# Performance work log

Hardware: AMD Instinct MI355X
Metric: run time of the kernel (lower is better)

Reference implementation:

```python
import jax, jax.numpy as jnp
import numpy as np

HUMAN_SIZE = 54
NUM_ACTIONS = 15
INPUT_SIZE = HUMAN_SIZE + NUM_ACTIONS  # 69
RNN_SIZE = 2048
BATCH = 512
SRC_LEN = 100
TGT_LEN = 50


def setup_inputs() -> dict:
    key = jax.random.key(0)
    ks = jax.random.split(key, 8)
    s = 1.0 / np.sqrt(RNN_SIZE)
    return {
        "encoder_inputs": jax.random.normal(ks[0], (BATCH, SRC_LEN, INPUT_SIZE), jnp.float32),
        "decoder_inputs": jax.random.normal(ks[1], (BATCH, TGT_LEN, INPUT_SIZE), jnp.float32),
        # GRUCell params (torch layout: weight_ih [3H, D], weight_hh [3H, H])
        "W_ih": jax.random.uniform(ks[2], (3 * RNN_SIZE, INPUT_SIZE), jnp.float32, -s, s),
        "W_hh": jax.random.uniform(ks[3], (3 * RNN_SIZE, RNN_SIZE), jnp.float32, -s, s),
        "b_ih": jax.random.uniform(ks[4], (3 * RNN_SIZE,), jnp.float32, -s, s),
        "b_hh": jax.random.uniform(ks[5], (3 * RNN_SIZE,), jnp.float32, -s, s),
        # fc1: Linear(rnn_size -> input_size)
        "fc1_w": jax.random.uniform(ks[6], (INPUT_SIZE, RNN_SIZE), jnp.float32, -s, s),
        "fc1_b": jax.random.uniform(ks[7], (INPUT_SIZE,), jnp.float32, -s, s),
    }


def _gru_cell(x, h, W_ih, W_hh, b_ih, b_hh):
    # torch.nn.GRUCell math
    gi = x @ W_ih.T + b_ih  # [B, 3H]
    gh = h @ W_hh.T + b_hh  # [B, 3H]
    i_r, i_z, i_n = jnp.split(gi, 3, axis=-1)
    h_r, h_z, h_n = jnp.split(gh, 3, axis=-1)
    r = jax.nn.sigmoid(i_r + h_r)
    z = jax.nn.sigmoid(i_z + h_z)
    n = jnp.tanh(i_n + r * h_n)
    return (1.0 - z) * n + z * h


def reference(encoder_inputs, decoder_inputs, W_ih, W_hh, b_ih, b_hh, fc1_w, fc1_b):
    B = encoder_inputs.shape[0]
    state0 = jnp.zeros((B, RNN_SIZE), encoder_inputs.dtype)

    # Encoder: source_seq_len - 1 steps (dropout p=0.0 -> identity)
    enc_t = jnp.swapaxes(encoder_inputs[:, : SRC_LEN - 1], 0, 1)  # [L-1, B, D]

    def enc_step(h, x):
        return _gru_cell(x, h, W_ih, W_hh, b_ih, b_hh), None

    state, _ = jax.lax.scan(enc_step, state0, enc_t)

    # (loop_function feeds the previous output back as the next input).
    def dec_step(carry, _):
        h, inp = carry
        inp = jax.lax.stop_gradient(inp)  # inp.detach() in torch
        h = _gru_cell(inp, h, W_ih, W_hh, b_ih, b_hh)
        out = inp + h @ fc1_w.T + fc1_b  # residual
        return (h, out), out

    (_, _), outs = jax.lax.scan(dec_step, (state, decoder_inputs[:, 0]), None, length=TGT_LEN)
    return jnp.swapaxes(outs, 0, 1)  # [B, TGT_LEN, INPUT_SIZE]
```

## Files before the change

kernel.cpp:

```cpp
#include <hip/hip_runtime.h>

#define KP   2176
#define H    2048
#define IN   69
#define TGT  50
#define NKT  68

typedef unsigned short ushort_t;
typedef unsigned int   uint_t;
typedef __attribute__((ext_vector_type(8))) short  short8;
typedef __attribute__((ext_vector_type(4))) float  float4_t;

#define MFMA_BF16 __builtin_amdgcn_mfma_f32_16x16x32_bf16

__device__ __forceinline__ ushort_t f2bf(float f) {
  union { float f; unsigned u; } v; v.f = f;
  unsigned u = v.u;
  return (ushort_t)((u + 0x7fffu + ((u >> 16) & 1u)) >> 16);
}

template <int N> __device__ __forceinline__ void waitv() {
  asm volatile("s_waitcnt vmcnt(%0)" :: "n"(N) : "memory");
}
#define LGKM0() asm volatile("s_waitcnt lgkmcnt(0)" ::: "memory")
#define SGB0()  __builtin_amdgcn_sched_barrier(0)
#define FENCE() asm volatile("" ::: "memory")

template <int OFF> __device__ __forceinline__ void gld(short8& d, uint_t voff, const void* base) {
  asm volatile("global_load_dwordx4 %0, %1, %2 offset:%3"
               : "=v"(d) : "v"(voff), "s"(base), "n"(OFF));
}


__global__ void build_w3(const float* __restrict__ Whh, const float* __restrict__ Wih,
                         ushort_t* __restrict__ W3) {
  int i = blockIdx.x * 256 + threadIdx.x;
  int lane = i & 63;
  int kt = (i >> 6) % NKT;
  int rb = i / (64 * NKT);
  int cb = rb / 3, g = rb - cb * 3;
  int c  = cb * 16 + (lane & 15);
  int gr = g * H + c;
  int k0 = kt * 32 + (lane >> 4) * 8;
  short8 v;
  #pragma unroll
  for (int j = 0; j < 8; ++j) {
    int k = k0 + j;
    float val = 0.f;
    if (k < H) val = Whh[(size_t)gr * H + k];
    else if (k < H + IN) val = Wih[(size_t)gr * IN + (k - H)];
    v[j] = (short)f2bf(val);
  }
  *(short8*)(W3 + (size_t)i * 8) = v;
}

__global__ void build_f2(const float* __restrict__ fc1w, ushort_t* __restrict__ F2) {
  int i = blockIdx.x * 256 + threadIdx.x;
  int lane = i & 63;
  int ni = (i >> 6) % 5;
  int kt = i / 320;
  int j  = ni * 16 + (lane & 15);
  int k0 = kt * 32 + (lane >> 4) * 8;
  short8 v;
  #pragma unroll
  for (int jj = 0; jj < 8; ++jj) {
    float val = (j < IN) ? fc1w[(size_t)j * H + k0 + jj] : 0.f;
    v[jj] = (short)f2bf(val);
  }
  *(short8*)(F2 + (size_t)i * 8) = v;
}

__global__ void zero_u4(uint4* p, int n) {
  int i = blockIdx.x * 256 + threadIdx.x;
  if (i < n) p[i] = make_uint4(0, 0, 0, 0);
}

__device__ __forceinline__ size_t a2_x_off(int b, int j) {
  int k = 2048 + j;
  int kt = k >> 5, kk = k & 31;
  int mb = b >> 4;
  int ln = (b & 15) | ((kk >> 3) << 4);
  return ((size_t)(mb * NKT + kt) * 64 + ln) * 16 + (kk & 7) * 2;
}

__global__ void fill_x0(const float* __restrict__ enc, char* __restrict__ A2) {
  int i = blockIdx.x * 256 + threadIdx.x;
  int b = i / IN, j = i - b * IN;
  *(ushort_t*)(A2 + a2_x_off(b, j)) = f2bf(enc[(size_t)b * 100 * IN + j]);
}

__global__ __launch_bounds__(256, 1) void gru_step(
    const char* __restrict__ Aprev, char* __restrict__ Anext,
    const char* __restrict__ W3p, float* __restrict__ h32,
    const float* __restrict__ bih, const float* __restrict__ bhh,
    const float* __restrict__ xsrc, int xstride)
{
  __shared__ short8  Aring[4][4][64];
  __shared__ ushort_t smh[64][72];
  __shared__ char ldspad[64000];

  const int tid = threadIdx.x;
  const int bid = blockIdx.x;
  const int lane = tid & 63, w = tid >> 6;
  const int l15 = lane & 15, l4 = lane >> 4;
  const int cg = (bid & 7) * 4 + ((bid >> 3) & 3);
  const int mt = bid >> 5;
  const int cb = cg * 4 + w;
  const int c  = cb * 16 + l15;

  if (xstride == -12345) ldspad[tid] = 1;

  const float br  = bih[c] + bhh[c];
  const float bz  = bih[H + c] + bhh[H + c];
  const float bin = bih[2 * H + c];
  const float bhn = bhh[2 * H + c];
  asm volatile("" :: "v"(br), "v"(bz), "v"(bin), "v"(bhn));

  const void* ApW = Aprev + (size_t)(mt * 4) * (NKT * 1024);
  uint_t vA  = (uint_t)(w * (NKT * 1024) + lane * 16);
  uint_t vB0 = (uint_t)((cb * 3 + 0) * (NKT * 1024) + lane * 16);
  uint_t vB1 = (uint_t)((cb * 3 + 1) * (NKT * 1024) + lane * 16);
  uint_t vB2 = (uint_t)((cb * 3 + 2) * (NKT * 1024) + lane * 16);

  short8 sa[4], fb[8][3];
  short8 fa0, fa1, fa2, fa3;
  float4_t acc[4][4] = {};

#define AISS(sl) { gld<0>(sa[sl], vA, ApW); vA += 1024; }
#define BISS(sl) { gld<0>(fb[sl][0], vB0, W3p); gld<0>(fb[sl][1], vB1, W3p); \
                   gld<0>(fb[sl][2], vB2, W3p); vB0 += 1024; vB1 += 1024; vB2 += 1024; }
#define MFMA3(mi, fav, j, G2) \
  acc[mi][0]  = MFMA_BF16(fav, fb[j][0], acc[mi][0], 0, 0, 0); \
  acc[mi][1]  = MFMA_BF16(fav, fb[j][1], acc[mi][1], 0, 0, 0); \
  acc[mi][G2] = MFMA_BF16(fav, fb[j][2], acc[mi][G2], 0, 0, 0);
#define MFMA12(j, G2) MFMA3(0, fa0, j, G2) MFMA3(1, fa1, j, G2) \
                      MFMA3(2, fa2, j, G2) MFMA3(3, fa3, j, G2)
#define RDFA(slot) \
  FENCE(); \
  fa0 = Aring[slot][0][lane]; fa1 = Aring[slot][1][lane]; \
  fa2 = Aring[slot][2][lane]; fa3 = Aring[slot][3][lane];

#define GRUT(u, G2) \
  AISS((u + 4) & 3) BISS((u + 7) & 7) \
  waitv<15>(); SGB0(); \
  Aring[(u + 1) & 3][w][lane] = sa[(u + 1) & 3]; \
  LGKM0(); \
  __builtin_amdgcn_s_barrier(); \
  RDFA(u & 3) \
  LGKM0(); SGB0(); \
  MFMA12(u, G2)

#define GRUTA(u, NW) \
  AISS((u + 4) & 3) \
  waitv<NW>(); SGB0(); \
  Aring[(u + 1) & 3][w][lane] = sa[(u + 1) & 3]; \
  LGKM0(); \
  __builtin_amdgcn_s_barrier(); \
  RDFA(u & 3) \
  LGKM0(); SGB0(); \
  MFMA12(u, 2)

#define GRUTN_W(u, NW, G2) \
  waitv<NW>(); SGB0(); \
  Aring[(u + 1) & 3][w][lane] = sa[(u + 1) & 3]; \
  LGKM0(); \
  __builtin_amdgcn_s_barrier(); \
  RDFA(u & 3) \
  LGKM0(); SGB0(); \
  MFMA12(u, G2)
#define GRUTN_NW(u, NW, G2) \
  waitv<NW>(); SGB0(); \
  LGKM0(); \
  __builtin_amdgcn_s_barrier(); \
  RDFA(u & 3) \
  LGKM0(); SGB0(); \
  MFMA12(u, G2)

  AISS(0) AISS(1) AISS(2) AISS(3)
  BISS(0) BISS(1) BISS(2) BISS(3) BISS(4) BISS(5) BISS(6)
  waitv<24>(); SGB0();
  Aring[0][w][lane] = sa[0];
  LGKM0();
  __builtin_amdgcn_s_barrier();

  #pragma unroll 1
  for (int g8 = 0; g8 < 7; ++g8) {
    GRUT(0, 2) GRUT(1, 2) GRUT(2, 2) GRUT(3, 2)
    GRUT(4, 2) GRUT(5, 2) GRUT(6, 2) GRUT(7, 2)
  }
  GRUT(0, 2) GRUT(1, 2) GRUT(2, 2) GRUT(3, 2) GRUT(4, 2)
  GRUTA(5, 12) GRUTA(6, 9) GRUTA(7, 6)
  GRUTN_W(0, 2, 3) GRUTN_W(1, 1, 3) GRUTN_W(2, 0, 3) GRUTN_NW(3, 0, 3)

  #pragma unroll
  for (int mi = 0; mi < 4; ++mi) {
    #pragma unroll
    for (int r4 = 0; r4 < 4; ++r4) {
      int m = mt * 64 + mi * 16 + l4 * 4 + r4;
      float rg = 1.f / (1.f + __expf(-(acc[mi][0][r4] + br)));
      float zg = 1.f / (1.f + __expf(-(acc[mi][1][r4] + bz)));
      float ng = tanhf(acc[mi][3][r4] + bin + rg * (acc[mi][2][r4] + bhn));
      float hold = h32[(size_t)m * H + c];
      float hn = (1.f - zg) * ng + zg * hold;
      h32[(size_t)m * H + c] = hn;
      smh[mi * 16 + l4 * 4 + r4][w * 16 + l15] = f2bf(hn);
    }
  }
  __syncthreads();
  #pragma unroll
  for (int e = 0; e < 2; ++e) {
    int cid = tid * 2 + e;
    int m = cid >> 3, ktrel = (cid >> 2) & 1, khi = cid & 3;
    short8 v = *(const short8*)&smh[m][ktrel * 32 + khi * 8];
    int m_abs = mt * 64 + m;
    int mb2 = m_abs >> 4;
    int ln = (m_abs & 15) | (khi << 4);
    int kt = cg * 2 + ktrel;
    *(short8*)(Anext + ((size_t)(mb2 * NKT + kt) * 64 + ln) * 16) = v;
  }
  if ((bid & 31) == 0 && xsrc != nullptr) {
    for (int i = tid; i < 64 * IN; i += 256) {
      int rr = i / IN, cc = i - rr * IN;
      int m = mt * 64 + rr;
      *(ushort_t*)(Anext + a2_x_off(m, cc)) = f2bf(xsrc[(size_t)m * xstride + cc]);
    }
  }
}

__global__ __launch_bounds__(256, 1) void out_step(
    char* __restrict__ Acat, const char* __restrict__ F2p,
    const float* __restrict__ fc1b, const float* __restrict__ inp,
    float* __restrict__ outp)
{
  __shared__ float4_t redf[4 * 5 * 64];
  const int tid = threadIdx.x;
  const int mb = blockIdx.x;
  const int lane = tid & 63, w = tid >> 6;
  const int l15 = lane & 15, l4 = lane >> 4;

  const void* F2b = (const char*)F2p + 4096;
  uint_t voA = (uint_t)((mb * NKT + w * 16) * 1024 + lane * 16);
  uint_t vf  = (uint_t)((w * 16) * 5120 + lane * 16);

  short8 da[8], db[8][5];
  float4_t oa[5] = {};

#define DPRO(sl) \
  gld<0>(da[sl], voA, Acat); \
  gld<0>(db[sl][0], vf, F2p); gld<1024>(db[sl][1], vf, F2p); \
  gld<2048>(db[sl][2], vf, F2p); gld<3072>(db[sl][3], vf, F2p); \
  gld<0>(db[sl][4], vf, F2b); \
  voA += 1024; vf += 5120;
#define DMM(sl) \
  { _Pragma("unroll") for (int nf = 0; nf < 5; ++nf) \
      oa[nf] = MFMA_BF16(da[sl], db[sl][nf], oa[nf], 0, 0, 0); }

  DPRO(0) DPRO(1) DPRO(2) DPRO(3) DPRO(4) DPRO(5) DPRO(6) DPRO(7)
  waitv<42>(); SGB0(); DMM(0) DPRO(0)
  waitv<42>(); SGB0(); DMM(1) DPRO(1)
  waitv<42>(); SGB0(); DMM(2) DPRO(2)
  waitv<42>(); SGB0(); DMM(3) DPRO(3)
  waitv<42>(); SGB0(); DMM(4) DPRO(4)
  waitv<42>(); SGB0(); DMM(5) DPRO(5)
  waitv<42>(); SGB0(); DMM(6) DPRO(6)
  waitv<42>(); SGB0(); DMM(7) DPRO(7)
  waitv<42>(); SGB0(); DMM(0)
  waitv<36>(); SGB0(); DMM(1)
  waitv<30>(); SGB0(); DMM(2)
  waitv<24>(); SGB0(); DMM(3)
  waitv<18>(); SGB0(); DMM(4)
  waitv<12>(); SGB0(); DMM(5)
  waitv<6>();  SGB0(); DMM(6)
  waitv<0>();  SGB0(); DMM(7)

  #pragma unroll
  for (int nf = 0; nf < 5; ++nf) redf[(w * 5 + nf) * 64 + lane] = oa[nf];
  __syncthreads();

  #pragma unroll 1
  for (int pass = 0; pass < 2; ++pass) {
    if (pass == 1 && w != 0) break;
    const int nf = pass ? 4 : w;
    float4_t sum = redf[(0 * 5 + nf) * 64 + lane] + redf[(1 * 5 + nf) * 64 + lane]
                 + redf[(2 * 5 + nf) * 64 + lane] + redf[(3 * 5 + nf) * 64 + lane];
    int j = nf * 16 + l15;
    if (j < IN) {
      float bj = fc1b[j];
      #pragma unroll
      for (int r4 = 0; r4 < 4; ++r4) {
        int m = mb * 16 + l4 * 4 + r4;
        float v = sum[r4] + bj + inp[(size_t)m * (TGT * IN) + j];
        outp[(size_t)m * (TGT * IN) + j] = v;
        *(ushort_t*)(Acat + a2_x_off(m, j)) = f2bf(v);
      }
    }
  }
}

extern "C" void kernel_launch(void* const* d_in, const int* in_sizes, int n_in,
                              void* d_out, int out_size, void* d_ws, size_t ws_size,
                              hipStream_t stream) {
  const float* enc  = (const float*)d_in[0];
  const float* dec  = (const float*)d_in[1];
  const float* Wih  = (const float*)d_in[2];
  const float* Whh  = (const float*)d_in[3];
  const float* b_ih = (const float*)d_in[4];
  const float* b_hh = (const float*)d_in[5];
  const float* fc1w = (const float*)d_in[6];
  const float* fc1b = (const float*)d_in[7];
  float* out = (float*)d_out;

  char* ws = (char*)d_ws;
  ushort_t* W3  = (ushort_t*)ws;
  char*     A0  = ws + 26738688;
  char*     A1  = ws + 28966912;
  float*    h32 = (float*)(ws + 31195136);
  ushort_t* F2  = (ushort_t*)(ws + 35389440);
  char* A2[2] = {A0, A1};

  build_w3<<<6528, 256, 0, stream>>>(Whh, Wih, W3);
  zero_u4<<<2112, 256, 0, stream>>>((uint4*)A0, 540672);
  fill_x0<<<138, 256, 0, stream>>>(enc, A0);
  build_f2<<<80, 256, 0, stream>>>(fc1w, F2);

  for (int t = 0; t < 149; ++t) {
    const float* xsrc = nullptr; int xstride = 0;
    if (t < 98)       { xsrc = enc + (size_t)(t + 1) * IN; xstride = 100 * IN; }
    else if (t == 98) { xsrc = dec;                        xstride = TGT * IN; }
    gru_step<<<256, 256, 0, stream>>>(A2[t & 1], A2[(t + 1) & 1], (const char*)W3, h32,
                                      b_ih, b_hh, xsrc, xstride);
    if (t >= 99) {
      int d = t - 99;
      const float* inp = (d == 0) ? dec : out + (size_t)(d - 1) * IN;
      out_step<<<32, 256, 0, stream>>>(A2[(t + 1) & 1], (const char*)F2, fc1b, inp,
                                       out + (size_t)d * IN);
    }
  }
}
```

Measured before the change: 4.024 ms.

## Split GRU step tiles across 512 blocks with 2x2 wave layout

Each block's output tile is halved to 32 columns by 64 rows, and the four waves are arranged 2x2, each doing two M-subtiles instead of four. The grid grows from 256 to 512 blocks so more compute units run each step. The large LDS padding that forced one block per CU is removed, so two blocks can now share a CU. The trade-off is that every A-tile load is now shared by fewer MFMAs, which raises A traffic per flop, and the per-block epilogue and x-fill mapping change to match.

```diff
diff --git a/kernel.cpp b/kernel.cpp
--- a/kernel.cpp
+++ b/kernel.cpp
@@ -96,19 +96,18 @@
     const float* __restrict__ xsrc, int xstride)
 {
   __shared__ short8  Aring[4][4][64];
-  __shared__ ushort_t smh[64][72];
-  __shared__ char ldspad[64000];
+  __shared__ ushort_t smh[64][36];
 
   const int tid = threadIdx.x;
   const int bid = blockIdx.x;
   const int lane = tid & 63, w = tid >> 6;
   const int l15 = lane & 15, l4 = lane >> 4;
-  const int cg = (bid & 7) * 4 + ((bid >> 3) & 3);
-  const int mt = bid >> 5;
-  const int cb = cg * 4 + w;
+  const int slot = bid >> 3;
+  const int cg = (bid & 7) * 8 + (slot & 7);
+  const int mt = slot >> 3;
+  const int wc = w & 1, wh = w >> 1;
+  const int cb = cg * 2 + wc;
   const int c  = cb * 16 + l15;
-
-  if (xstride == -12345) ldspad[tid] = 1;
 
   const float br  = bih[c] + bhh[c];
   const float bz  = bih[H + c] + bhh[H + c];
@@ -123,8 +122,8 @@
   uint_t vB2 = (uint_t)((cb * 3 + 2) * (NKT * 1024) + lane * 16);
 
   short8 sa[4], fb[8][3];
-  short8 fa0, fa1, fa2, fa3;
-  float4_t acc[4][4] = {};
+  short8 fa0, fa1;
+  float4_t acc[2][4] = {};
 
 #define AISS(sl) { gld<0>(sa[sl], vA, ApW); vA += 1024; }
 #define BISS(sl) { gld<0>(fb[sl][0], vB0, W3p); gld<0>(fb[sl][1], vB1, W3p); \
@@ -133,12 +132,10 @@
   acc[mi][0]  = MFMA_BF16(fav, fb[j][0], acc[mi][0], 0, 0, 0); \
   acc[mi][1]  = MFMA_BF16(fav, fb[j][1], acc[mi][1], 0, 0, 0); \
   acc[mi][G2] = MFMA_BF16(fav, fb[j][2], acc[mi][G2], 0, 0, 0);
-#define MFMA12(j, G2) MFMA3(0, fa0, j, G2) MFMA3(1, fa1, j, G2) \
-                      MFMA3(2, fa2, j, G2) MFMA3(3, fa3, j, G2)
-#define RDFA(slot) \
+#define MFMA6(j, G2) MFMA3(0, fa0, j, G2) MFMA3(1, fa1, j, G2)
+#define RDFA(ss) \
   FENCE(); \
-  fa0 = Aring[slot][0][lane]; fa1 = Aring[slot][1][lane]; \
-  fa2 = Aring[slot][2][lane]; fa3 = Aring[slot][3][lane];
+  fa0 = Aring[ss][wh * 2][lane]; fa1 = Aring[ss][wh * 2 + 1][lane];
 
 #define GRUT(u, G2) \
   AISS((u + 4) & 3) BISS((u + 7) & 7) \
@@ -148,7 +145,7 @@
   __builtin_amdgcn_s_barrier(); \
   RDFA(u & 3) \
   LGKM0(); SGB0(); \
-  MFMA12(u, G2)
+  MFMA6(u, G2)
 
 #define GRUTA(u, NW) \
   AISS((u + 4) & 3) \
@@ -158,7 +155,7 @@
   __builtin_amdgcn_s_barrier(); \
   RDFA(u & 3) \
   LGKM0(); SGB0(); \
-  MFMA12(u, 2)
+  MFMA6(u, 2)
 
 #define GRUTN_W(u, NW, G2) \
   waitv<NW>(); SGB0(); \
@@ -167,14 +164,14 @@
   __builtin_amdgcn_s_barrier(); \
   RDFA(u & 3) \
   LGKM0(); SGB0(); \
-  MFMA12(u, G2)
+  MFMA6(u, G2)
 #define GRUTN_NW(u, NW, G2) \
   waitv<NW>(); SGB0(); \
   LGKM0(); \
   __builtin_amdgcn_s_barrier(); \
   RDFA(u & 3) \
   LGKM0(); SGB0(); \
-  MFMA12(u, G2)
+  MFMA6(u, G2)
 
   AISS(0) AISS(1) AISS(2) AISS(3)
   BISS(0) BISS(1) BISS(2) BISS(3) BISS(4) BISS(5) BISS(6)
@@ -193,32 +190,30 @@
   GRUTN_W(0, 2, 3) GRUTN_W(1, 1, 3) GRUTN_W(2, 0, 3) GRUTN_NW(3, 0, 3)
 
   #pragma unroll
-  for (int mi = 0; mi < 4; ++mi) {
+  for (int mi = 0; mi < 2; ++mi) {
     #pragma unroll
     for (int r4 = 0; r4 < 4; ++r4) {
-      int m = mt * 64 + mi * 16 + l4 * 4 + r4;
+      int mloc = (wh * 2 + mi) * 16 + l4 * 4 + r4;
+      int m = mt * 64 + mloc;
       float rg = 1.f / (1.f + __expf(-(acc[mi][0][r4] + br)));
       float zg = 1.f / (1.f + __expf(-(acc[mi][1][r4] + bz)));
       float ng = tanhf(acc[mi][3][r4] + bin + rg * (acc[mi][2][r4] + bhn));
       float hold = h32[(size_t)m * H + c];
       float hn = (1.f - zg) * ng + zg * hold;
       h32[(size_t)m * H + c] = hn;
-      smh[mi * 16 + l4 * 4 + r4][w * 16 + l15] = f2bf(hn);
+      smh[mloc][wc * 16 + l15] = f2bf(hn);
     }
   }
   __syncthreads();
-  #pragma unroll
-  for (int e = 0; e < 2; ++e) {
-    int cid = tid * 2 + e;
-    int m = cid >> 3, ktrel = (cid >> 2) & 1, khi = cid & 3;
-    short8 v = *(const short8*)&smh[m][ktrel * 32 + khi * 8];
-    int m_abs = mt * 64 + m;
+  {
+    int mloc = tid >> 2, khi = tid & 3;
+    short8 v = *(const short8*)&smh[mloc][khi * 8];
+    int m_abs = mt * 64 + mloc;
     int mb2 = m_abs >> 4;
     int ln = (m_abs & 15) | (khi << 4);
-    int kt = cg * 2 + ktrel;
-    *(short8*)(Anext + ((size_t)(mb2 * NKT + kt) * 64 + ln) * 16) = v;
-  }
-  if ((bid & 31) == 0 && xsrc != nullptr) {
+    *(short8*)(Anext + ((size_t)(mb2 * NKT + cg) * 64 + ln) * 16) = v;
+  }
+  if (cg == 0 && xsrc != nullptr) {
     for (int i = tid; i < 64 * IN; i += 256) {
       int rr = i / IN, cc = i - rr * IN;
       int m = mt * 64 + rr;
@@ -327,7 +322,7 @@
     const float* xsrc = nullptr; int xstride = 0;
     if (t < 98)       { xsrc = enc + (size_t)(t + 1) * IN; xstride = 100 * IN; }
     else if (t == 98) { xsrc = dec;                        xstride = TGT * IN; }
-    gru_step<<<256, 256, 0, stream>>>(A2[t & 1], A2[(t + 1) & 1], (const char*)W3, h32,
+    gru_step<<<512, 256, 0, stream>>>(A2[t & 1], A2[(t + 1) & 1], (const char*)W3, h32,
                                       b_ih, b_hh, xsrc, xstride);
     if (t >= 99) {
       int d = t - 99;
```

New measurement: 4.111 ms. +2.1%, slower.

## Fuse all GRU and output steps into one persistent kernel with grid barriers

Applied to the files above, without the earlier changes.

Replaces the 199 per-step kernel launches with a single persistent kernel of 256 blocks that loops over all timesteps and syncs with an atomic-counter grid barrier. The hidden state now lives in registers instead of a global fp32 buffer, and the output projection runs in the first 32 blocks after each barrier. Cross-block data goes through cache-bypassing sc0/sc1 loads and stores. This removes launch overhead and the h32 global traffic, but adds spin-wait barrier cost and needs all 256 blocks to be resident together.

```diff
diff --git a/kernel.cpp b/kernel.cpp
--- a/kernel.cpp
+++ b/kernel.cpp
@@ -30,7 +30,22 @@
   asm volatile("global_load_dwordx4 %0, %1, %2 offset:%3"
                : "=v"(d) : "v"(voff), "s"(base), "n"(OFF));
 }
-
+template <int OFF> __device__ __forceinline__ void gld_sc(short8& d, uint_t voff, const void* base) {
+  asm volatile("global_load_dwordx4 %0, %1, %2 offset:%3 sc0 sc1"
+               : "=v"(d) : "v"(voff), "s"(base), "n"(OFF));
+}
+__device__ __forceinline__ void st128_sc(void* addr, short8 v) {
+  asm volatile("global_store_dwordx4 %0, %1, off sc0 sc1" :: "v"(addr), "v"(v) : "memory");
+}
+__device__ __forceinline__ void st16_sc(void* addr, uint_t v) {
+  asm volatile("global_store_short %0, %1, off sc0 sc1" :: "v"(addr), "v"(v) : "memory");
+}
+__device__ __forceinline__ void st32_sc(void* addr, float v) {
+  asm volatile("global_store_dword %0, %1, off sc0 sc1" :: "v"(addr), "v"(v) : "memory");
+}
+__device__ __forceinline__ void ld32_sc_nw(float& d, const void* addr) {
+  asm volatile("global_load_dword %0, %1, off sc0 sc1" : "=v"(d) : "v"(addr) : "memory");
+}
 
 __global__ void build_w3(const float* __restrict__ Whh, const float* __restrict__ Wih,
                          ushort_t* __restrict__ W3) {
@@ -89,15 +104,15 @@
   *(ushort_t*)(A2 + a2_x_off(b, j)) = f2bf(enc[(size_t)b * 100 * IN + j]);
 }
 
-__global__ __launch_bounds__(256, 1) void gru_step(
-    const char* __restrict__ Aprev, char* __restrict__ Anext,
-    const char* __restrict__ W3p, float* __restrict__ h32,
+__global__ __launch_bounds__(256, 1) void persist(
+    const char* __restrict__ W3p, char* A0, char* A1, const char* __restrict__ F2p,
+    const float* __restrict__ enc, const float* __restrict__ dec,
     const float* __restrict__ bih, const float* __restrict__ bhh,
-    const float* __restrict__ xsrc, int xstride)
+    const float* __restrict__ fc1b, float* __restrict__ out, int* barcnt)
 {
-  __shared__ short8  Aring[4][4][64];
-  __shared__ ushort_t smh[64][72];
-  __shared__ char ldspad[64000];
+  __shared__ __align__(16) char ldsraw[25600];
+  short8  (*Aring)[4][64] = (short8 (*)[4][64])ldsraw;
+  ushort_t (*smh)[72]     = (ushort_t (*)[72])(ldsraw + 16384);
 
   const int tid = threadIdx.x;
   const int bid = blockIdx.x;
@@ -108,25 +123,52 @@
   const int cb = cg * 4 + w;
   const int c  = cb * 16 + l15;
 
-  if (xstride == -12345) ldspad[tid] = 1;
-
   const float br  = bih[c] + bhh[c];
   const float bz  = bih[H + c] + bhh[H + c];
   const float bin = bih[2 * H + c];
   const float bhn = bhh[2 * H + c];
   asm volatile("" :: "v"(br), "v"(bz), "v"(bin), "v"(bhn));
 
-  const void* ApW = Aprev + (size_t)(mt * 4) * (NKT * 1024);
-  uint_t vA  = (uint_t)(w * (NKT * 1024) + lane * 16);
-  uint_t vB0 = (uint_t)((cb * 3 + 0) * (NKT * 1024) + lane * 16);
-  uint_t vB1 = (uint_t)((cb * 3 + 1) * (NKT * 1024) + lane * 16);
-  uint_t vB2 = (uint_t)((cb * 3 + 2) * (NKT * 1024) + lane * 16);
-
-  short8 sa[4], fb[8][3];
-  short8 fa0, fa1, fa2, fa3;
-  float4_t acc[4][4] = {};
-
-#define AISS(sl) { gld<0>(sa[sl], vA, ApW); vA += 1024; }
+  float hreg[4][4] = {};
+
+  const uint_t vAi  = (uint_t)(w * (NKT * 1024) + lane * 16);
+  const uint_t vB0i = (uint_t)((cb * 3 + 0) * (NKT * 1024) + lane * 16);
+  const uint_t vB1i = vB0i + (uint_t)(NKT * 1024);
+  const uint_t vB2i = vB1i + (uint_t)(NKT * 1024);
+
+  int epoch = 0;
+  auto gbar = [&]() {
+    asm volatile("s_waitcnt vmcnt(0) lgkmcnt(0)" ::: "memory");
+    __builtin_amdgcn_s_barrier();
+    ++epoch;
+    if (tid == 0) {
+      atomicAdd(barcnt, 1);
+      const int tgt = epoch * 256;
+      int v = 0;
+      for (int it = 0; it < 20000000; ++it) {
+        asm volatile("global_load_dword %0, %1, off sc0 sc1\n\ts_waitcnt vmcnt(0)"
+                     : "=v"(v) : "v"((const int*)barcnt) : "memory");
+        if (v >= tgt) break;
+        __builtin_amdgcn_s_sleep(2);
+      }
+    }
+    __builtin_amdgcn_s_barrier();
+  };
+
+  #pragma unroll 1
+  for (int t = 0; t < 149; ++t) {
+    char* Ain  = (t & 1) ? A1 : A0;
+    char* Aout = (t & 1) ? A0 : A1;
+    const void* ApW = Ain + (size_t)(mt * 4) * (NKT * 1024);
+
+    uint_t vA = vAi;
+    uint_t vB0 = vB0i, vB1 = vB1i, vB2 = vB2i;
+
+    short8 sa[4], fb[8][3];
+    short8 fa0, fa1, fa2, fa3;
+    float4_t acc[4][4] = {};
+
+#define AISS(sl) { gld_sc<0>(sa[sl], vA, ApW); vA += 1024; }
 #define BISS(sl) { gld<0>(fb[sl][0], vB0, W3p); gld<0>(fb[sl][1], vB1, W3p); \
                    gld<0>(fb[sl][2], vB2, W3p); vB0 += 1024; vB1 += 1024; vB2 += 1024; }
 #define MFMA3(mi, fav, j, G2) \
@@ -135,11 +177,10 @@
   acc[mi][G2] = MFMA_BF16(fav, fb[j][2], acc[mi][G2], 0, 0, 0);
 #define MFMA12(j, G2) MFMA3(0, fa0, j, G2) MFMA3(1, fa1, j, G2) \
                       MFMA3(2, fa2, j, G2) MFMA3(3, fa3, j, G2)
-#define RDFA(slot) \
+#define RDFA(ss) \
   FENCE(); \
-  fa0 = Aring[slot][0][lane]; fa1 = Aring[slot][1][lane]; \
-  fa2 = Aring[slot][2][lane]; fa3 = Aring[slot][3][lane];
-
+  fa0 = Aring[ss][0][lane]; fa1 = Aring[ss][1][lane]; \
+  fa2 = Aring[ss][2][lane]; fa3 = Aring[ss][3][lane];
 #define GRUT(u, G2) \
   AISS((u + 4) & 3) BISS((u + 7) & 7) \
   waitv<15>(); SGB0(); \
@@ -149,7 +190,6 @@
   RDFA(u & 3) \
   LGKM0(); SGB0(); \
   MFMA12(u, G2)
-
 #define GRUTA(u, NW) \
   AISS((u + 4) & 3) \
   waitv<NW>(); SGB0(); \
@@ -159,7 +199,6 @@
   RDFA(u & 3) \
   LGKM0(); SGB0(); \
   MFMA12(u, 2)
-
 #define GRUTN_W(u, NW, G2) \
   waitv<NW>(); SGB0(); \
   Aring[(u + 1) & 3][w][lane] = sa[(u + 1) & 3]; \
@@ -176,123 +215,135 @@
   LGKM0(); SGB0(); \
   MFMA12(u, G2)
 
-  AISS(0) AISS(1) AISS(2) AISS(3)
-  BISS(0) BISS(1) BISS(2) BISS(3) BISS(4) BISS(5) BISS(6)
-  waitv<24>(); SGB0();
-  Aring[0][w][lane] = sa[0];
-  LGKM0();
-  __builtin_amdgcn_s_barrier();
-
-  #pragma unroll 1
-  for (int g8 = 0; g8 < 7; ++g8) {
-    GRUT(0, 2) GRUT(1, 2) GRUT(2, 2) GRUT(3, 2)
-    GRUT(4, 2) GRUT(5, 2) GRUT(6, 2) GRUT(7, 2)
-  }
-  GRUT(0, 2) GRUT(1, 2) GRUT(2, 2) GRUT(3, 2) GRUT(4, 2)
-  GRUTA(5, 12) GRUTA(6, 9) GRUTA(7, 6)
-  GRUTN_W(0, 2, 3) GRUTN_W(1, 1, 3) GRUTN_W(2, 0, 3) GRUTN_NW(3, 0, 3)
-
-  #pragma unroll
-  for (int mi = 0; mi < 4; ++mi) {
+    AISS(0) AISS(1) AISS(2) AISS(3)
+    BISS(0) BISS(1) BISS(2) BISS(3) BISS(4) BISS(5) BISS(6)
+    waitv<24>(); SGB0();
+    Aring[0][w][lane] = sa[0];
+    LGKM0();
+    __builtin_amdgcn_s_barrier();
+
+    #pragma unroll 1
+    for (int g8 = 0; g8 < 7; ++g8) {
+      GRUT(0, 2) GRUT(1, 2) GRUT(2, 2) GRUT(3, 2)
+      GRUT(4, 2) GRUT(5, 2) GRUT(6, 2) GRUT(7, 2)
+    }
+    GRUT(0, 2) GRUT(1, 2) GRUT(2, 2) GRUT(3, 2) GRUT(4, 2)
+    GRUTA(5, 12) GRUTA(6, 9) GRUTA(7, 6)
+    GRUTN_W(0, 2, 3) GRUTN_W(1, 1, 3) GRUTN_W(2, 0, 3) GRUTN_NW(3, 0, 3)
+
     #pragma unroll
-    for (int r4 = 0; r4 < 4; ++r4) {
-      int m = mt * 64 + mi * 16 + l4 * 4 + r4;
-      float rg = 1.f / (1.f + __expf(-(acc[mi][0][r4] + br)));
-      float zg = 1.f / (1.f + __expf(-(acc[mi][1][r4] + bz)));
-      float ng = tanhf(acc[mi][3][r4] + bin + rg * (acc[mi][2][r4] + bhn));
-      float hold = h32[(size_t)m * H + c];
-      float hn = (1.f - zg) * ng + zg * hold;
-      h32[(size_t)m * H + c] = hn;
-      smh[mi * 16 + l4 * 4 + r4][w * 16 + l15] = f2bf(hn);
-    }
-  }
-  __syncthreads();
-  #pragma unroll
-  for (int e = 0; e < 2; ++e) {
-    int cid = tid * 2 + e;
-    int m = cid >> 3, ktrel = (cid >> 2) & 1, khi = cid & 3;
-    short8 v = *(const short8*)&smh[m][ktrel * 32 + khi * 8];
-    int m_abs = mt * 64 + m;
-    int mb2 = m_abs >> 4;
-    int ln = (m_abs & 15) | (khi << 4);
-    int kt = cg * 2 + ktrel;
-    *(short8*)(Anext + ((size_t)(mb2 * NKT + kt) * 64 + ln) * 16) = v;
-  }
-  if ((bid & 31) == 0 && xsrc != nullptr) {
-    for (int i = tid; i < 64 * IN; i += 256) {
-      int rr = i / IN, cc = i - rr * IN;
-      int m = mt * 64 + rr;
-      *(ushort_t*)(Anext + a2_x_off(m, cc)) = f2bf(xsrc[(size_t)m * xstride + cc]);
-    }
-  }
-}
-
-__global__ __launch_bounds__(256, 1) void out_step(
-    char* __restrict__ Acat, const char* __restrict__ F2p,
-    const float* __restrict__ fc1b, const float* __restrict__ inp,
-    float* __restrict__ outp)
-{
-  __shared__ float4_t redf[4 * 5 * 64];
-  const int tid = threadIdx.x;
-  const int mb = blockIdx.x;
-  const int lane = tid & 63, w = tid >> 6;
-  const int l15 = lane & 15, l4 = lane >> 4;
-
-  const void* F2b = (const char*)F2p + 4096;
-  uint_t voA = (uint_t)((mb * NKT + w * 16) * 1024 + lane * 16);
-  uint_t vf  = (uint_t)((w * 16) * 5120 + lane * 16);
-
-  short8 da[8], db[8][5];
-  float4_t oa[5] = {};
-
-#define DPRO(sl) \
-  gld<0>(da[sl], voA, Acat); \
-  gld<0>(db[sl][0], vf, F2p); gld<1024>(db[sl][1], vf, F2p); \
-  gld<2048>(db[sl][2], vf, F2p); gld<3072>(db[sl][3], vf, F2p); \
-  gld<0>(db[sl][4], vf, F2b); \
-  voA += 1024; vf += 5120;
-#define DMM(sl) \
-  { _Pragma("unroll") for (int nf = 0; nf < 5; ++nf) \
-      oa[nf] = MFMA_BF16(da[sl], db[sl][nf], oa[nf], 0, 0, 0); }
-
-  DPRO(0) DPRO(1) DPRO(2) DPRO(3) DPRO(4) DPRO(5) DPRO(6) DPRO(7)
-  waitv<42>(); SGB0(); DMM(0) DPRO(0)
-  waitv<42>(); SGB0(); DMM(1) DPRO(1)
-  waitv<42>(); SGB0(); DMM(2) DPRO(2)
-  waitv<42>(); SGB0(); DMM(3) DPRO(3)
-  waitv<42>(); SGB0(); DMM(4) DPRO(4)
-  waitv<42>(); SGB0(); DMM(5) DPRO(5)
-  waitv<42>(); SGB0(); DMM(6) DPRO(6)
-  waitv<42>(); SGB0(); DMM(7) DPRO(7)
-  waitv<42>(); SGB0(); DMM(0)
-  waitv<36>(); SGB0(); DMM(1)
-  waitv<30>(); SGB0(); DMM(2)
-  waitv<24>(); SGB0(); DMM(3)
-  waitv<18>(); SGB0(); DMM(4)
-  waitv<12>(); SGB0(); DMM(5)
-  waitv<6>();  SGB0(); DMM(6)
-  waitv<0>();  SGB0(); DMM(7)
-
-  #pragma unroll
-  for (int nf = 0; nf < 5; ++nf) redf[(w * 5 + nf) * 64 + lane] = oa[nf];
-  __syncthreads();
-
-  #pragma unroll 1
-  for (int pass = 0; pass < 2; ++pass) {
-    if (pass == 1 && w != 0) break;
-    const int nf = pass ? 4 : w;
-    float4_t sum = redf[(0 * 5 + nf) * 64 + lane] + redf[(1 * 5 + nf) * 64 + lane]
-                 + redf[(2 * 5 + nf) * 64 + lane] + redf[(3 * 5 + nf) * 64 + lane];
-    int j = nf * 16 + l15;
-    if (j < IN) {
-      float bj = fc1b[j];
+    for (int mi = 0; mi < 4; ++mi) {
       #pragma unroll
       for (int r4 = 0; r4 < 4; ++r4) {
-        int m = mb * 16 + l4 * 4 + r4;
-        float v = sum[r4] + bj + inp[(size_t)m * (TGT * IN) + j];
-        outp[(size_t)m * (TGT * IN) + j] = v;
-        *(ushort_t*)(Acat + a2_x_off(m, j)) = f2bf(v);
+        float rg = 1.f / (1.f + __expf(-(acc[mi][0][r4] + br)));
+        float zg = 1.f / (1.f + __expf(-(acc[mi][1][r4] + bz)));
+        float ng = tanhf(acc[mi][3][r4] + bin + rg * (acc[mi][2][r4] + bhn));
+        float hn = (1.f - zg) * ng + zg * hreg[mi][r4];
+        hreg[mi][r4] = hn;
+        smh[mi * 16 + l4 * 4 + r4][w * 16 + l15] = f2bf(hn);
       }
+    }
+    __syncthreads();
+    #pragma unroll
+    for (int e = 0; e < 2; ++e) {
+      int cid = tid * 2 + e;
+      int m = cid >> 3, ktrel = (cid >> 2) & 1, khi = cid & 3;
+      short8 v = *(const short8*)&smh[m][ktrel * 32 + khi * 8];
+      int m_abs = mt * 64 + m;
+      int mb2 = m_abs >> 4;
+      int ln = (m_abs & 15) | (khi << 4);
+      int kt = cg * 2 + ktrel;
+      st128_sc(Aout + ((size_t)(mb2 * NKT + kt) * 64 + ln) * 16, v);
+    }
+    if ((bid & 31) == 0 && t < 99) {
+      const float* xs = (t < 98) ? (enc + (size_t)(t + 1) * IN) : dec;
+      const int xstride = (t < 98) ? 100 * IN : TGT * IN;
+      for (int i = tid; i < 64 * IN; i += 256) {
+        int rr = i / IN, cc = i - rr * IN;
+        int m = mt * 64 + rr;
+        st16_sc(Aout + a2_x_off(m, cc), (uint_t)f2bf(xs[(size_t)m * xstride + cc]));
+      }
+    }
+    gbar();
+
+    if (t >= 99) {
+      if (bid < 32) {
+        const int d = t - 99;
+        const int mbo = bid;
+        float4_t* redf = (float4_t*)ldsraw;
+        const void* F2b = (const char*)F2p + 4096;
+        uint_t voA = (uint_t)((mbo * NKT + w * 16) * 1024 + lane * 16);
+        uint_t vf  = (uint_t)((w * 16) * 5120 + lane * 16);
+        short8 da[8], db[8][5];
+        float4_t oa[5] = {};
+
+#define DPRO(sl) \
+        gld_sc<0>(da[sl], voA, Aout); \
+        gld<0>(db[sl][0], vf, F2p); gld<1024>(db[sl][1], vf, F2p); \
+        gld<2048>(db[sl][2], vf, F2p); gld<3072>(db[sl][3], vf, F2p); \
+        gld<0>(db[sl][4], vf, F2b); \
+        voA += 1024; vf += 5120;
+#define DMM(sl) \
+        { _Pragma("unroll") for (int nf = 0; nf < 5; ++nf) \
+            oa[nf] = MFMA_BF16(da[sl], db[sl][nf], oa[nf], 0, 0, 0); }
+
+        DPRO(0) DPRO(1) DPRO(2) DPRO(3) DPRO(4) DPRO(5) DPRO(6) DPRO(7)
+        waitv<42>(); SGB0(); DMM(0) DPRO(0)
+        waitv<42>(); SGB0(); DMM(1) DPRO(1)
+        waitv<42>(); SGB0(); DMM(2) DPRO(2)
+        waitv<42>(); SGB0(); DMM(3) DPRO(3)
+        waitv<42>(); SGB0(); DMM(4) DPRO(4)
+        waitv<42>(); SGB0(); DMM(5) DPRO(5)
+        waitv<42>(); SGB0(); DMM(6) DPRO(6)
+        waitv<42>(); SGB0(); DMM(7) DPRO(7)
+        waitv<42>(); SGB0(); DMM(0)
+        waitv<36>(); SGB0(); DMM(1)
+        waitv<30>(); SGB0(); DMM(2)
+        waitv<24>(); SGB0(); DMM(3)
+        waitv<18>(); SGB0(); DMM(4)
+        waitv<12>(); SGB0(); DMM(5)
+        waitv<6>();  SGB0(); DMM(6)
+        waitv<0>();  SGB0(); DMM(7)
+
+        #pragma unroll
+        for (int nf = 0; nf < 5; ++nf) redf[(w * 5 + nf) * 64 + lane] = oa[nf];
+        __syncthreads();
+
+        #pragma unroll 1
+        for (int pass = 0; pass < 2; ++pass) {
+          if (pass == 1 && w != 0) break;
+          const int nf = pass ? 4 : w;
+          float4_t sum = redf[(0 * 5 + nf) * 64 + lane] + redf[(1 * 5 + nf) * 64 + lane]
+                       + redf[(2 * 5 + nf) * 64 + lane] + redf[(3 * 5 + nf) * 64 + lane];
+          int j = nf * 16 + l15;
+          if (j < IN) {
+            float bj = fc1b[j];
+            float iv0, iv1, iv2, iv3;
+            if (d == 0) {
+              iv0 = dec[(size_t)(mbo * 16 + l4 * 4 + 0) * (TGT * IN) + j];
+              iv1 = dec[(size_t)(mbo * 16 + l4 * 4 + 1) * (TGT * IN) + j];
+              iv2 = dec[(size_t)(mbo * 16 + l4 * 4 + 2) * (TGT * IN) + j];
+              iv3 = dec[(size_t)(mbo * 16 + l4 * 4 + 3) * (TGT * IN) + j];
+            } else {
+              const float* pv = out + (size_t)(d - 1) * IN + j;
+              ld32_sc_nw(iv0, pv + (size_t)(mbo * 16 + l4 * 4 + 0) * (TGT * IN));
+              ld32_sc_nw(iv1, pv + (size_t)(mbo * 16 + l4 * 4 + 1) * (TGT * IN));
+              ld32_sc_nw(iv2, pv + (size_t)(mbo * 16 + l4 * 4 + 2) * (TGT * IN));
+              ld32_sc_nw(iv3, pv + (size_t)(mbo * 16 + l4 * 4 + 3) * (TGT * IN));
+              waitv<0>(); SGB0();
+            }
+            float ivv[4] = {iv0, iv1, iv2, iv3};
+            #pragma unroll
+            for (int r4 = 0; r4 < 4; ++r4) {
+              int m = mbo * 16 + l4 * 4 + r4;
+              float v = sum[r4] + bj + ivv[r4];
+              st32_sc(out + (size_t)m * (TGT * IN) + (size_t)d * IN + j, v);
+              st16_sc(Aout + a2_x_off(m, j), (uint_t)f2bf(v));
+            }
+          }
+        }
+      }
+      gbar();
     }
   }
 }
@@ -314,26 +365,14 @@
   ushort_t* W3  = (ushort_t*)ws;
   char*     A0  = ws + 26738688;
   char*     A1  = ws + 28966912;
-  float*    h32 = (float*)(ws + 31195136);
-  ushort_t* F2  = (ushort_t*)(ws + 35389440);
-  char* A2[2] = {A0, A1};
+  int*      bar = (int*)(ws + 31195136);
+  ushort_t* F2  = (ushort_t*)(ws + 31196160);
 
   build_w3<<<6528, 256, 0, stream>>>(Whh, Wih, W3);
-  zero_u4<<<2112, 256, 0, stream>>>((uint4*)A0, 540672);
+  zero_u4<<<1089, 256, 0, stream>>>((uint4*)A0, 278592);
   fill_x0<<<138, 256, 0, stream>>>(enc, A0);
   build_f2<<<80, 256, 0, stream>>>(fc1w, F2);
 
-  for (int t = 0; t < 149; ++t) {
-    const float* xsrc = nullptr; int xstride = 0;
-    if (t < 98)       { xsrc = enc + (size_t)(t + 1) * IN; xstride = 100 * IN; }
-    else if (t == 98) { xsrc = dec;                        xstride = TGT * IN; }
-    gru_step<<<256, 256, 0, stream>>>(A2[t & 1], A2[(t + 1) & 1], (const char*)W3, h32,
-                                      b_ih, b_hh, xsrc, xstride);
-    if (t >= 99) {
-      int d = t - 99;
-      const float* inp = (d == 0) ? dec : out + (size_t)(d - 1) * IN;
-      out_step<<<32, 256, 0, stream>>>(A2[(t + 1) & 1], (const char*)F2, fc1b, inp,
-                                       out + (size_t)d * IN);
-    }
-  }
-}
+  persist<<<256, 256, 0, stream>>>((const char*)W3, A0, A1, (const char*)F2,
+                                   enc, dec, b_ih, b_hh, fc1b, out, bar);
+}
```

Measured after the change: 4.307 ms. 1.07x slower.
